# Performance work log

Hardware: AMD Instinct MI355X
Metric: run time of the kernel (lower is better)

Reference implementation:

```python
import jax, jax.numpy as jnp
import numpy as np
import math

N_HEAD = 12
BLOCK = 256  # local attention block size (ls)
EPS = 1e-6


def _rotate(x):
    # pairs (a, b) -> (-b, a) over last dim (matches rotate_embeddings)
    a = x[..., 0::2]
    b = x[..., 1::2]
    return jnp.stack([-b, a], axis=-1).reshape(x.shape)


def setup_inputs() -> dict:
    key = jax.random.key(0)
    k1, k2, k3 = jax.random.split(key, 3)
    B, T, C = 4, 8192, 768
    s = 0.02
    return {
        "x": jax.random.normal(k1, (B, T, C), jnp.float32),
        "w_qkv": jax.random.normal(k2, (C, 3 * C), jnp.float32) * s,
        "w_ln": jnp.ones((C,), jnp.float32),
        "w_proj": jax.random.normal(k3, (C, C), jnp.float32) * s,
    }


def reference(x, w_qkv, w_ln, w_proj):
    B, T, C = x.shape
    nh, ls = N_HEAD, BLOCK
    hd = C // nh
    ng = T // ls

    xb = x.reshape(B, ng, ls, C)
    qkv = xb @ w_qkv                                   # (B,ng,ls,3C)
    q, k, v = jnp.split(qkv, 3, axis=-1)

    # QK RMSNorm over full embedding dim (before head split)
    def rms(t):
        return t * jax.lax.rsqrt(jnp.mean(t * t, axis=-1, keepdims=True) + EPS) * w_ln
    q, k = rms(q), rms(k)

    # split heads: (B,ng,nh,ls,hd)
    def heads(t):
        return jnp.swapaxes(t.reshape(B, ng, ls, nh, hd), 2, 3)
    q, k, v = heads(q), heads(k), heads(v)

    # RoPE (repo layout: freqs tiled via cat((ts,ts)), interleaved pair rotation)
    pos = 10000.0 ** ((-2.0 * jnp.arange(0, hd, 2, dtype=jnp.float32) - 1.0) / hd)
    ts = jnp.arange(ls, dtype=jnp.float32)[:, None] * pos[None, :]   # (ls, hd/2)
    rot = jnp.concatenate([ts, ts], axis=-1)                          # (ls, hd)
    cos, sin = jnp.cos(rot), jnp.sin(rot)
    q = q * cos + _rotate(q) * sin
    k = k * cos + _rotate(k) * sin

    # block-causal scores: causal only within each local block
    scale = 1.0 / math.sqrt(hd)
    att = jnp.einsum('bgnqd,bgnkd->bgnqk', q, k) * scale              # (B,ng,nh,ls,ls)
    mask = jnp.tril(jnp.ones((ls, ls), dtype=bool))
    att = jnp.where(mask, att, -jnp.finfo(att.dtype).max)
    att = jax.nn.softmax(att, axis=-1)
    y = jnp.einsum('bgnqk,bgnkd->bgnqd', att, v)                      # (B,ng,nh,ls,hd)

    y = jnp.swapaxes(y, 2, 3).reshape(B, ng, ls, C)
    y = y @ w_proj
    return y.reshape(B, T, C)
```

## Files before the change

kernel.cpp:

```cpp
#include <hip/hip_runtime.h>
#include <math.h>

typedef __attribute__((ext_vector_type(8))) short bf16x8;
typedef __attribute__((ext_vector_type(4))) short bf16x4;
typedef __attribute__((ext_vector_type(2))) short bf16x2;
typedef __attribute__((ext_vector_type(4))) float f32x4;
typedef __attribute__((ext_vector_type(16))) float f32x16;

#define NH 12
#define HD 64
#define C0 768
#define C3 2304
#define LS 256
#define KT12 12

static __device__ __forceinline__ float bf2f(short u) {
  union { unsigned int i; float f; } c;
  c.i = ((unsigned int)(unsigned short)u) << 16;
  return c.f;
}
static __device__ __forceinline__ short f2bf(float f) {
  union { float f; unsigned int i; } c; c.f = f;
  unsigned int x = c.i;
  x += 0x7fffu + ((x >> 16) & 1u);
  return (short)(x >> 16);
}
static __device__ __forceinline__ unsigned pk2(float a, float b) {
  return (unsigned)(unsigned short)f2bf(a) | ((unsigned)(unsigned short)f2bf(b) << 16);
}

static __device__ __forceinline__ void gload_lds16(const short* g, const short* l) {
  unsigned long long ga = (unsigned long long)g;
  unsigned int la = (unsigned int)(unsigned long long)l;
  __builtin_amdgcn_global_load_lds(
      (const __attribute__((address_space(1))) void*)ga,
      (__attribute__((address_space(3))) void*)la, 16, 0, 0);
}

__global__ __launch_bounds__(256) void cast_kernel(const float* __restrict__ in,
                                                   short* __restrict__ out, int nquads) {
  int i = blockIdx.x * blockDim.x + threadIdx.x;
  int stride = gridDim.x * blockDim.x;
  for (; i < nquads; i += stride) {
    float4 v = ((const float4*)in)[i];
    bf16x4 o = { f2bf(v.x), f2bf(v.y), f2bf(v.z), f2bf(v.w) };
    ((bf16x4*)out)[i] = o;
  }
}

template <int WNG>
__global__ __launch_bounds__(256) void cast_pack_B_kernel(const float* __restrict__ w,
                                                          short* __restrict__ Bpk, int N) {
  __shared__ short sb[WNG * 64 * 64];
  int bn = blockIdx.x, kt = blockIdx.y, t = threadIdx.x;
#pragma unroll
  for (int i = 0; i < WNG * 2; ++i) {
    int seg = i * 256 + t;
    int k = seg / (WNG * 8);
    int nc = (seg % (WNG * 8)) * 8;
    const float* src = w + ((long)(kt * 64 + k)) * N + bn * (WNG * 64) + nc;
    float4 v0 = *(const float4*)src;
    float4 v1 = *(const float4*)(src + 4);
    sb[(nc + 0) * 64 + k] = f2bf(v0.x); sb[(nc + 1) * 64 + k] = f2bf(v0.y);
    sb[(nc + 2) * 64 + k] = f2bf(v0.z); sb[(nc + 3) * 64 + k] = f2bf(v0.w);
    sb[(nc + 4) * 64 + k] = f2bf(v1.x); sb[(nc + 5) * 64 + k] = f2bf(v1.y);
    sb[(nc + 6) * 64 + k] = f2bf(v1.z); sb[(nc + 7) * 64 + k] = f2bf(v1.w);
  }
  __syncthreads();
#pragma unroll
  for (int i = 0; i < WNG * 2; ++i) {
    int c = i * 256 + t;
    int l = c & 63, f = c >> 6;
    int ks = f & 3, nt = (f >> 2) & 1, wng = f >> 3;
    int col = wng * 64 + nt * 32 + (l & 31);
    int kk = ks * 16 + (l >> 5) * 8;
    bf16x8 v = *(bf16x8*)&sb[col * 64 + kk];
    *(bf16x8*)&Bpk[(((long)bn * KT12 + kt) * (WNG * 512) + c) * 8] = v;
  }
}

__global__ void rope_tab_kernel(float* __restrict__ cost, float* __restrict__ sint) {
  int t = blockIdx.x, d = threadIdx.x;
  int i = d & 31;
  float freq = powf(10000.0f, -(float)(4 * i + 1) / 64.0f);
  float th = (float)t * freq;
  cost[t * 64 + d] = cosf(th);
  sint[t * 64 + d] = sinf(th);
}

#define PH_OPEN                                        \
  __builtin_amdgcn_s_barrier();                        \
  asm volatile("s_waitcnt lgkmcnt(0)" ::: "memory");   \
  __builtin_amdgcn_sched_barrier(0);                   \
  __builtin_amdgcn_s_setprio(1);
#define PH_MID __builtin_amdgcn_s_setprio(0);
#define PH_CLOSE                                       \
  asm volatile("s_waitcnt vmcnt(2)" ::: "memory");     \
  __builtin_amdgcn_s_barrier();
#define MM8(ASET, BSET, MP, NT)                                                     \
  { _Pragma("unroll") for (int m2_ = 0; m2_ < 2; ++m2_)                             \
      _Pragma("unroll") for (int ks_ = 0; ks_ < 4; ++ks_)                           \
        acc[(MP)*2 + m2_][NT] = __builtin_amdgcn_mfma_f32_32x32x16_bf16(            \
            ASET[m2_ * 4 + ks_], BSET[ks_], acc[(MP)*2 + m2_][NT], 0, 0, 0); }

template <int OUT_F32, int PACKED_A>
__global__ __launch_bounds__(512, 2) void gemm32_kernel(const short* __restrict__ Apk,
                                                        const short* __restrict__ Bpk,
                                                        const short* __restrict__ Arm,
                                                        void* __restrict__ Cout,
                                                        int N, int K, int nbn) {
  __shared__ short lds[65536];
  int t = threadIdx.x, lane = t & 63, wave = t >> 6;
  int wm = (wave >> 2) * 128, wng = wave & 3, wn = wng * 64, mh = wave >> 2;
  int id = blockIdx.x;
  int cpx = gridDim.x >> 3;
  int sw = (id & 7) * cpx + (id >> 3);
  int bm = sw / nbn, bn = sw % nbn;

  f32x16 acc[4][2];
#pragma unroll
  for (int m = 0; m < 4; ++m)
#pragma unroll
    for (int n = 0; n < 2; ++n)
#pragma unroll
      for (int r = 0; r < 16; ++r) acc[m][n][r] = 0.f;

  bf16x8 a0[8], a1[8], b0[4], b1[4];

  auto STAGE = [&](int s) {
    if (s >= 4 * KT12) return;
    int q = s & 3, Ts = s >> 2;
    int bb = (Ts & 1) * 32768;
    if (q < 2) {
      if (PACKED_A) {
        int c = q * 1024 + t;
        const short* src = Apk + ((long)bm * KT12 + Ts) * 16384 + (long)c * 8;
        gload_lds16(src, &lds[bb + c * 8]);
        gload_lds16(src + 4096, &lds[bb + (c + 512) * 8]);
      } else {
        int row = q * 128 + (t >> 3);
        int cr = q * 1024 + t;
        const short* s1 = Arm + ((long)(bm * 256 + row)) * K + Ts * 64 + ((t & 7) ^ (row & 7)) * 8;
        gload_lds16(s1, &lds[bb + cr * 8]);
        int row2 = row + 64;
        const short* s2 = Arm + ((long)(bm * 256 + row2)) * K + Ts * 64 + ((t & 7) ^ (row2 & 7)) * 8;
        gload_lds16(s2, &lds[bb + (cr + 512) * 8]);
      }
    } else {
      int c = (q - 2) * 1024 + t;
      const short* src = Bpk + ((long)bn * KT12 + Ts) * 16384 + (long)c * 8;
      gload_lds16(src, &lds[bb + 16384 + c * 8]);
      gload_lds16(src + 4096, &lds[bb + 16384 + (c + 512) * 8]);
    }
  };
  auto LDA = [&](bf16x8* d, int b, int mhalf) {
    if (PACKED_A) {
#pragma unroll
      for (int m2 = 0; m2 < 2; ++m2)
#pragma unroll
        for (int ks = 0; ks < 4; ++ks)
          d[m2 * 4 + ks] =
              *(bf16x8*)&lds[b * 32768 + ((mh * 16 + (mhalf * 2 + m2) * 4 + ks) * 64 + lane) * 8];
    } else {
#pragma unroll
      for (int m2 = 0; m2 < 2; ++m2)
#pragma unroll
        for (int ks = 0; ks < 4; ++ks) {
          int row = wm + (mhalf * 2 + m2) * 32 + (lane & 31);
          int g = (ks * 2 + (lane >> 5)) ^ (row & 7);
          d[m2 * 4 + ks] = *(bf16x8*)&lds[b * 32768 + row * 64 + g * 8];
        }
    }
  };
  auto LDB = [&](bf16x8* d, int b, int nt) {
#pragma unroll
    for (int ks = 0; ks < 4; ++ks)
      d[ks] = *(bf16x8*)&lds[b * 32768 + 16384 + ((wng * 8 + nt * 4 + ks) * 64 + lane) * 8];
  };

  for (int s = 0; s < 7; ++s) STAGE(s);
  asm volatile("s_waitcnt vmcnt(6)" ::: "memory");
  __builtin_amdgcn_s_barrier();
  LDA(a0, 0, 0);
  LDB(b0, 0, 0);
  LDB(b1, 0, 1);

  for (int it = 0; it < KT12 / 2; ++it) {
    int P0 = 8 * it;
    PH_OPEN; MM8(a0, b0, 0, 0); PH_MID;
    LDA(a1, 0, 1); STAGE(P0 + 7); PH_CLOSE;
    PH_OPEN; MM8(a0, b1, 0, 1); PH_MID;
    LDA(a0, 1, 0); STAGE(P0 + 8); PH_CLOSE;
    PH_OPEN; MM8(a1, b0, 1, 0); PH_MID;
    LDB(b0, 1, 0); STAGE(P0 + 9); PH_CLOSE;
    PH_OPEN; MM8(a1, b1, 1, 1); PH_MID;
    LDB(b1, 1, 1); STAGE(P0 + 10); PH_CLOSE;
    PH_OPEN; MM8(a0, b0, 0, 0); PH_MID;
    LDA(a1, 1, 1); STAGE(P0 + 11); PH_CLOSE;
    PH_OPEN; MM8(a0, b1, 0, 1); PH_MID;
    LDA(a0, 0, 0); STAGE(P0 + 12); PH_CLOSE;
    PH_OPEN; MM8(a1, b0, 1, 0); PH_MID;
    LDB(b0, 0, 0); STAGE(P0 + 13); PH_CLOSE;
    PH_OPEN; MM8(a1, b1, 1, 1); PH_MID;
    LDB(b1, 0, 1); STAGE(P0 + 14); PH_CLOSE;
  }

  long crow0 = (long)bm * 256 + wm;
  long ccol0 = (long)bn * 256 + wn;
  int rbase = 4 * (lane >> 5);
  int cl = lane & 31;
#pragma unroll
  for (int mt = 0; mt < 4; ++mt)
#pragma unroll
    for (int nt = 0; nt < 2; ++nt)
#pragma unroll
      for (int reg = 0; reg < 16; ++reg) {
        long row = crow0 + mt * 32 + (reg & 3) + 8 * (reg >> 2) + rbase;
        long col = ccol0 + nt * 32 + cl;
        float v = acc[mt][nt][reg];
        if (OUT_F32) ((float*)Cout)[row * N + col] = v;
        else ((short*)Cout)[row * N + col] = f2bf(v);
      }
}

template <int OUT_F32>
__global__ __launch_bounds__(256, 2) void gemm128_kernel(const short* __restrict__ Arm,
                                                         const short* __restrict__ Bpk,
                                                         void* __restrict__ Cout,
                                                         int N, int K, int nbn) {
  __shared__ short lds[32768];
  int t = threadIdx.x, lane = t & 63, wave = t >> 6;
  int wm = (wave >> 1) * 64, wng = wave & 1;
  int id = blockIdx.x;
  int cpx = gridDim.x >> 3;
  int sw = (id & 7) * cpx + (id >> 3);
  int bm = sw / nbn, bn = sw % nbn;
  int l31 = lane & 31, lh = lane >> 5;

  f32x16 acc[2][2];
#pragma unroll
  for (int m = 0; m < 2; ++m)
#pragma unroll
    for (int n = 0; n < 2; ++n)
#pragma unroll
      for (int r = 0; r < 16; ++r) acc[m][n][r] = 0.f;

  auto STAGE = [&](int T) {
    int bb = (T & 1) * 16384;
#pragma unroll
    for (int i = 0; i < 4; ++i) {
      int q = i * 256 + t;
      int row = q >> 3, cp = q & 7;
      const short* ga = Arm + ((long)(bm * 128 + row)) * K + T * 64 + ((cp ^ (row & 7)) * 8);
      gload_lds16(ga, &lds[bb + q * 8]);
      const short* gb = Bpk + ((long)bn * KT12 + T) * 8192 + (long)q * 8;
      gload_lds16(gb, &lds[bb + 8192 + q * 8]);
    }
  };

  STAGE(0);
  asm volatile("s_waitcnt vmcnt(0)" ::: "memory");
  __builtin_amdgcn_s_barrier();

  for (int T = 0; T < KT12; ++T) {
    int bb = (T & 1) * 16384;
    if (T + 1 < KT12) STAGE(T + 1);
    bf16x8 a[2][4], b[2][4];
#pragma unroll
    for (int mt = 0; mt < 2; ++mt) {
      int row = wm + mt * 32 + l31;
      int s8 = row & 7;
#pragma unroll
      for (int ks = 0; ks < 4; ++ks) {
        int g = (ks * 2 + lh) ^ s8;
        a[mt][ks] = *(bf16x8*)&lds[bb + row * 64 + g * 8];
      }
    }
#pragma unroll
    for (int nt = 0; nt < 2; ++nt)
#pragma unroll
      for (int ks = 0; ks < 4; ++ks)
        b[nt][ks] = *(bf16x8*)&lds[bb + 8192 + (((wng * 2 + nt) * 4 + ks) * 64 + lane) * 8];
    __builtin_amdgcn_s_setprio(1);
#pragma unroll
    for (int mt = 0; mt < 2; ++mt)
#pragma unroll
      for (int nt = 0; nt < 2; ++nt)
#pragma unroll
        for (int ks = 0; ks < 4; ++ks)
          acc[mt][nt] = __builtin_amdgcn_mfma_f32_32x32x16_bf16(a[mt][ks], b[nt][ks],
                                                                acc[mt][nt], 0, 0, 0);
    __builtin_amdgcn_s_setprio(0);
    asm volatile("s_waitcnt lgkmcnt(0)" ::: "memory");
    asm volatile("s_waitcnt vmcnt(0)" ::: "memory");
    __builtin_amdgcn_s_barrier();
  }

  long crow0 = (long)bm * 128 + wm;
  long ccol0 = (long)bn * 128 + wng * 64;
  int rbase = 4 * lh;
#pragma unroll
  for (int mt = 0; mt < 2; ++mt)
#pragma unroll
    for (int nt = 0; nt < 2; ++nt)
#pragma unroll
      for (int reg = 0; reg < 16; ++reg) {
        long row = crow0 + mt * 32 + (reg & 3) + 8 * (reg >> 2) + rbase;
        long col = ccol0 + nt * 32 + l31;
        float v = acc[mt][nt][reg];
        if (OUT_F32) ((float*)Cout)[row * N + col] = v;
        else ((short*)Cout)[row * N + col] = f2bf(v);
      }
}

__global__ __launch_bounds__(384) void norm_rope_kernel(short* __restrict__ QKV,
    const float* __restrict__ w_ln, const float* __restrict__ cost,
    const float* __restrict__ sint) {
  int row = blockIdx.x;
  int t = row & 255;
  int i = threadIdx.x;
  bool isq = i < 192;
  int e0 = (i - (isq ? 0 : 192)) * 4;
  long off = (long)row * C3 + (isq ? 0 : C0) + e0;
  bf16x4 v4 = *(const bf16x4*)&QKV[off];
  float a = bf2f(v4.x), b = bf2f(v4.y), c = bf2f(v4.z), d = bf2f(v4.w);
  float ss = a * a + b * b + c * c + d * d;
#pragma unroll
  for (int o = 32; o > 0; o >>= 1) ss += __shfl_down(ss, o);
  __shared__ float red[6];
  if ((i & 63) == 0) red[i >> 6] = ss;
  __syncthreads();
  float s3 = isq ? (red[0] + red[1] + red[2]) : (red[3] + red[4] + red[5]);
  float r = rsqrtf(s3 * (1.0f / 768.0f) + 1e-6f);
  float4 wl = *(const float4*)&w_ln[e0];
  int d0 = e0 & 63;
  float4 cs = *(const float4*)&cost[t * 64 + d0];
  float4 sn = *(const float4*)&sint[t * 64 + d0];
  float n0 = a * r * wl.x, n1 = b * r * wl.y, n2 = c * r * wl.z, n3 = d * r * wl.w;
  bf16x4 o;
  o.x = f2bf(n0 * cs.x - n1 * sn.x);
  o.y = f2bf(n1 * cs.y + n0 * sn.y);
  o.z = f2bf(n2 * cs.z - n3 * sn.z);
  o.w = f2bf(n3 * cs.w + n2 * sn.w);
  *(bf16x4*)&QKV[off] = o;
}

__global__ __launch_bounds__(512, 3) void attn_kernel(const short* __restrict__ QKV,
                                                      short* __restrict__ Y) {
  __shared__ short Ks[256 * 64];
  __shared__ short Vt[64 * 256];
  int blk = blockIdx.x;
  int bg = blk / NH, h = blk % NH;
  const long base = (long)bg * LS * C3 + h * HD;
  int tid = threadIdx.x, lane = tid & 63, wave = tid >> 6;
  int lr = lane & 15, lg = lane >> 4;

#pragma unroll
  for (int it = 0; it < 4; ++it) {
    int q = it * 512 + tid;
    int row = q >> 3, cp = q & 7;
    int gcp = cp ^ (row & 7);
    gload_lds16(QKV + base + (long)row * C3 + C0 + gcp * 8, &Ks[q * 8]);
  }
#pragma unroll
  for (int it = 0; it < 8; ++it) {
    int e = tid * 4 + it * 2048;
    int k = e >> 6, n = e & 63;
    bf16x4 v = *(const bf16x4*)&QKV[base + (long)k * C3 + 2 * C0 + n];
#pragma unroll
    for (int j = 0; j < 4; ++j) {
      int nn = n + j;
      Vt[nn * 256 + (((k >> 3) ^ (nn & 7)) << 3) + (k & 7)] = v[j];
    }
  }
  asm volatile("s_waitcnt vmcnt(0)" ::: "memory");
  __syncthreads();

  int addrA = (((lane >> 4) & 1) * 32 + lr) * 4;
  int addrB = addrA + 64;
  bool selhi = (lane & 32) != 0;

  for (int tt = 0; tt < 2; ++tt) {
    int tile = (tt == 0) ? wave : (15 - wave);
    int m0 = tile * 16;
    bf16x8 qf[2];
#pragma unroll
    for (int ks = 0; ks < 2; ++ks)
      qf[ks] = *(const bf16x8*)&QKV[base + (long)(m0 + lr) * C3 + ks * 32 + lg * 8];

    f32x4 zero4 = {0.f, 0.f, 0.f, 0.f};
    f32x4 accs[16];
#pragma unroll
    for (int n = 0; n < 16; ++n) accs[n] = zero4;

    __builtin_amdgcn_s_setprio(1);
#pragma unroll
    for (int n = 0; n < 16; ++n) {
      if (n <= tile) {
        int row = n * 16 + lr, sw = row & 7;
        bf16x8 k0 = *(bf16x8*)&Ks[row * 64 + ((lg ^ sw) << 3)];
        bf16x8 k1 = *(bf16x8*)&Ks[row * 64 + (((4 + lg) ^ sw) << 3)];
        accs[n] = __builtin_amdgcn_mfma_f32_16x16x32_bf16(k0, qf[0], accs[n], 0, 0, 0);
        accs[n] = __builtin_amdgcn_mfma_f32_16x16x32_bf16(k1, qf[1], accs[n], 0, 0, 0);
      }
    }
    __builtin_amdgcn_s_setprio(0);

    float tm[16];
#pragma unroll
    for (int n = 0; n < 16; ++n) {
      if (n <= tile) {
        if (n == tile) {
#pragma unroll
          for (int r = 0; r < 4; ++r)
            accs[n][r] = (lg * 4 + r <= lr) ? accs[n][r] : -1e30f;
        }
        float m01 = fmaxf(accs[n][0], accs[n][1]);
        float m23 = fmaxf(accs[n][2], accs[n][3]);
        tm[n] = fmaxf(m01, m23);
      } else {
        tm[n] = -1e30f;
      }
    }
#pragma unroll
    for (int st = 1; st < 16; st <<= 1)
#pragma unroll
      for (int j = 0; j < 16; j += 2 * st) tm[j] = fmaxf(tm[j], tm[j + st]);
    float mloc = tm[0];
    mloc = fmaxf(mloc, __shfl_xor(mloc, 16));
    mloc = fmaxf(mloc, __shfl_xor(mloc, 32));

    float ts[16];
#pragma unroll
    for (int n = 0; n < 16; ++n) {
      if (n <= tile) {
#pragma unroll
        for (int r = 0; r < 4; ++r) accs[n][r] = __expf((accs[n][r] - mloc) * 0.125f);
        float s01 = accs[n][0] + accs[n][1];
        float s23 = accs[n][2] + accs[n][3];
        ts[n] = s01 + s23;
      } else {
        ts[n] = 0.f;
      }
    }
#pragma unroll
    for (int st = 1; st < 16; st <<= 1)
#pragma unroll
      for (int j = 0; j < 16; j += 2 * st) ts[j] += ts[j + st];
    float s = ts[0];
    s += __shfl_xor(s, 16);
    s += __shfl_xor(s, 32);
    float rs = 1.0f / s;
    float rv[4];
#pragma unroll
    for (int r = 0; r < 4; ++r) {
      union { float f; int i; } c; c.f = rs;
      union { int i; float f; } o;
      o.i = __builtin_amdgcn_ds_bpermute((lg * 4 + r) * 4, c.i);
      rv[r] = o.f;
    }

    int ktmax = (m0 + 15) >> 5;
    f32x4 yacc[4];
#pragma unroll
    for (int n2 = 0; n2 < 4; ++n2) yacc[n2] = zero4;
#pragma unroll
    for (int kt = 0; kt < 8; ++kt) {
      if (kt <= ktmax) {
        int n0 = 2 * kt, n1 = 2 * kt + 1;
        unsigned a01_0 = pk2(accs[n0][0], accs[n0][1]);
        unsigned a23_0 = pk2(accs[n0][2], accs[n0][3]);
        unsigned a01_1 = (n1 <= tile) ? pk2(accs[n1][0], accs[n1][1]) : 0u;
        unsigned a23_1 = (n1 <= tile) ? pk2(accs[n1][2], accs[n1][3]) : 0u;
        union { unsigned u[4]; bf16x8 v; } af;
        unsigned g0a = (unsigned)__builtin_amdgcn_ds_bpermute(addrA, (int)a01_0);
        unsigned g0b = (unsigned)__builtin_amdgcn_ds_bpermute(addrA, (int)a01_1);
        unsigned g1a = (unsigned)__builtin_amdgcn_ds_bpermute(addrA, (int)a23_0);
        unsigned g1b = (unsigned)__builtin_amdgcn_ds_bpermute(addrA, (int)a23_1);
        unsigned g2a = (unsigned)__builtin_amdgcn_ds_bpermute(addrB, (int)a01_0);
        unsigned g2b = (unsigned)__builtin_amdgcn_ds_bpermute(addrB, (int)a01_1);
        unsigned g3a = (unsigned)__builtin_amdgcn_ds_bpermute(addrB, (int)a23_0);
        unsigned g3b = (unsigned)__builtin_amdgcn_ds_bpermute(addrB, (int)a23_1);
        af.u[0] = selhi ? g0b : g0a;
        af.u[1] = selhi ? g1b : g1a;
        af.u[2] = selhi ? g2b : g2a;
        af.u[3] = selhi ? g3b : g3a;
        int ac = kt * 32 + lg * 8;
        __builtin_amdgcn_s_setprio(1);
#pragma unroll
        for (int n2 = 0; n2 < 4; ++n2) {
          int vn = n2 * 16 + lr;
          bf16x8 vb = *(bf16x8*)&Vt[vn * 256 + (((ac >> 3) ^ (vn & 7)) << 3)];
          yacc[n2] = __builtin_amdgcn_mfma_f32_16x16x32_bf16(af.v, vb, yacc[n2], 0, 0, 0);
        }
        __builtin_amdgcn_s_setprio(0);
      }
    }

#pragma unroll
    for (int n2 = 0; n2 < 4; ++n2) {
#pragma unroll
      for (int r = 0; r < 4; ++r) {
        int row = m0 + lg * 4 + r, d = n2 * 16 + lr;
        Y[((long)(bg * LS + row)) * C0 + h * HD + d] = f2bf(yacc[n2][r] * rv[r]);
      }
    }
  }
}

extern "C" void kernel_launch(void* const* d_in, const int* in_sizes, int n_in,
                              void* d_out, int out_size, void* d_ws, size_t ws_size,
                              hipStream_t stream) {
  (void)in_sizes; (void)n_in; (void)out_size; (void)ws_size;
  const float* x = (const float*)d_in[0];
  const float* w_qkv = (const float*)d_in[1];
  const float* w_ln = (const float*)d_in[2];
  const float* w_proj = (const float*)d_in[3];
  float* out = (float*)d_out;

  char* ws = (char*)d_ws;
  short* Xb      = (short*)(ws + 0);
  short* QKV     = (short*)(ws + 50331648);
  short* Yb      = (short*)(ws + 201326592);
  short* WqkvPk  = (short*)(ws + 251658240);
  short* WprojPk = (short*)(ws + 255197184);
  float* cost    = (float*)(ws + 256376832);
  float* sint    = (float*)(ws + 256442368);

  cast_kernel<<<2048, 256, 0, stream>>>(x, Xb, (4 * 8192 * C0) / 4);
  cast_pack_B_kernel<4><<<dim3(9, KT12), 256, 0, stream>>>(w_qkv, WqkvPk, C3);
  cast_pack_B_kernel<2><<<dim3(6, KT12), 256, 0, stream>>>(w_proj, WprojPk, C0);
  rope_tab_kernel<<<256, 64, 0, stream>>>(cost, sint);

  gemm32_kernel<0, 0><<<128 * 9, 512, 0, stream>>>(nullptr, WqkvPk, Xb, QKV,
                                                   C3, C0, 9);
  norm_rope_kernel<<<32768, 384, 0, stream>>>(QKV, w_ln, cost, sint);
  attn_kernel<<<128 * NH, 512, 0, stream>>>(QKV, Yb);
  gemm128_kernel<1><<<256 * 6, 256, 0, stream>>>(Yb, WprojPk, out, C0, C0, 6);
}
```

Measured before the change: 372.0 us.

## Pre-pack activation tiles into MFMA fragment layout and re-swizzle V transpose

Replaces the plain fp32-to-bf16 cast of x with a kernel that casts and repacks each 256x64 tile into the MFMA fragment order, so the QKV GEMM uses the packed-A path with contiguous LDS loads instead of swizzled row-major loads. The attention kernel now loads V with 16-byte vectors and uses an XOR swizzle that also mixes in the high bits of the column index, aiming to reduce LDS bank conflicts on the transposed V writes. The cast pass gains an LDS round trip, and the packed layout ties A to this tile shape.

New measurement: 362.9 us. 1.03x faster.

```diff
diff --git a/kernel.cpp b/kernel.cpp
--- a/kernel.cpp
+++ b/kernel.cpp
@@ -37,14 +37,31 @@
       (__attribute__((address_space(3))) void*)la, 16, 0, 0);
 }
 
-__global__ __launch_bounds__(256) void cast_kernel(const float* __restrict__ in,
-                                                   short* __restrict__ out, int nquads) {
-  int i = blockIdx.x * blockDim.x + threadIdx.x;
-  int stride = gridDim.x * blockDim.x;
-  for (; i < nquads; i += stride) {
-    float4 v = ((const float4*)in)[i];
-    bf16x4 o = { f2bf(v.x), f2bf(v.y), f2bf(v.z), f2bf(v.w) };
-    ((bf16x4*)out)[i] = o;
+__global__ __launch_bounds__(256) void cast_pack_A_kernel(const float* __restrict__ x,
+                                                          short* __restrict__ Apk) {
+  __shared__ short sb[256 * 64];
+  int bm = blockIdx.x, kt = blockIdx.y, t = threadIdx.x;
+#pragma unroll
+  for (int i = 0; i < 8; ++i) {
+    int seg = i * 256 + t;
+    int row = seg >> 3, sc8 = seg & 7;
+    const float* src = x + ((long)(bm * 256 + row)) * C0 + kt * 64 + sc8 * 8;
+    float4 v0 = *(const float4*)src;
+    float4 v1 = *(const float4*)(src + 4);
+    bf16x8 o = { f2bf(v0.x), f2bf(v0.y), f2bf(v0.z), f2bf(v0.w),
+                 f2bf(v1.x), f2bf(v1.y), f2bf(v1.z), f2bf(v1.w) };
+    *(bf16x8*)&sb[row * 64 + ((sc8 ^ (row & 7)) << 3)] = o;
+  }
+  __syncthreads();
+#pragma unroll
+  for (int i = 0; i < 8; ++i) {
+    int c = i * 256 + t;
+    int l = c & 63, f = c >> 6;
+    int ks = f & 3, mt = (f >> 2) & 3, mh = f >> 4;
+    int row = mh * 128 + mt * 32 + (l & 31);
+    int kc = ks * 2 + (l >> 5);
+    bf16x8 v = *(bf16x8*)&sb[row * 64 + ((kc ^ (row & 7)) << 3)];
+    *(bf16x8*)&Apk[(((long)bm * KT12 + kt) * 2048 + c) * 8] = v;
   }
 }
 
@@ -103,10 +120,9 @@
         acc[(MP)*2 + m2_][NT] = __builtin_amdgcn_mfma_f32_32x32x16_bf16(            \
             ASET[m2_ * 4 + ks_], BSET[ks_], acc[(MP)*2 + m2_][NT], 0, 0, 0); }
 
-template <int OUT_F32, int PACKED_A>
+template <int OUT_F32>
 __global__ __launch_bounds__(512, 2) void gemm32_kernel(const short* __restrict__ Apk,
                                                         const short* __restrict__ Bpk,
-                                                        const short* __restrict__ Arm,
                                                         void* __restrict__ Cout,
                                                         int N, int K, int nbn) {
   __shared__ short lds[65536];
@@ -132,20 +148,10 @@
     int q = s & 3, Ts = s >> 2;
     int bb = (Ts & 1) * 32768;
     if (q < 2) {
-      if (PACKED_A) {
-        int c = q * 1024 + t;
-        const short* src = Apk + ((long)bm * KT12 + Ts) * 16384 + (long)c * 8;
-        gload_lds16(src, &lds[bb + c * 8]);
-        gload_lds16(src + 4096, &lds[bb + (c + 512) * 8]);
-      } else {
-        int row = q * 128 + (t >> 3);
-        int cr = q * 1024 + t;
-        const short* s1 = Arm + ((long)(bm * 256 + row)) * K + Ts * 64 + ((t & 7) ^ (row & 7)) * 8;
-        gload_lds16(s1, &lds[bb + cr * 8]);
-        int row2 = row + 64;
-        const short* s2 = Arm + ((long)(bm * 256 + row2)) * K + Ts * 64 + ((t & 7) ^ (row2 & 7)) * 8;
-        gload_lds16(s2, &lds[bb + (cr + 512) * 8]);
-      }
+      int c = q * 1024 + t;
+      const short* src = Apk + ((long)bm * KT12 + Ts) * 16384 + (long)c * 8;
+      gload_lds16(src, &lds[bb + c * 8]);
+      gload_lds16(src + 4096, &lds[bb + (c + 512) * 8]);
     } else {
       int c = (q - 2) * 1024 + t;
       const short* src = Bpk + ((long)bn * KT12 + Ts) * 16384 + (long)c * 8;
@@ -154,23 +160,12 @@
     }
   };
   auto LDA = [&](bf16x8* d, int b, int mhalf) {
-    if (PACKED_A) {
-#pragma unroll
-      for (int m2 = 0; m2 < 2; ++m2)
-#pragma unroll
-        for (int ks = 0; ks < 4; ++ks)
-          d[m2 * 4 + ks] =
-              *(bf16x8*)&lds[b * 32768 + ((mh * 16 + (mhalf * 2 + m2) * 4 + ks) * 64 + lane) * 8];
-    } else {
-#pragma unroll
-      for (int m2 = 0; m2 < 2; ++m2)
-#pragma unroll
-        for (int ks = 0; ks < 4; ++ks) {
-          int row = wm + (mhalf * 2 + m2) * 32 + (lane & 31);
-          int g = (ks * 2 + (lane >> 5)) ^ (row & 7);
-          d[m2 * 4 + ks] = *(bf16x8*)&lds[b * 32768 + row * 64 + g * 8];
-        }
-    }
+#pragma unroll
+    for (int m2 = 0; m2 < 2; ++m2)
+#pragma unroll
+      for (int ks = 0; ks < 4; ++ks)
+        d[m2 * 4 + ks] =
+            *(bf16x8*)&lds[b * 32768 + ((mh * 16 + (mhalf * 2 + m2) * 4 + ks) * 64 + lane) * 8];
   };
   auto LDB = [&](bf16x8* d, int b, int nt) {
 #pragma unroll
@@ -363,14 +358,15 @@
     gload_lds16(QKV + base + (long)row * C3 + C0 + gcp * 8, &Ks[q * 8]);
   }
 #pragma unroll
-  for (int it = 0; it < 8; ++it) {
-    int e = tid * 4 + it * 2048;
+  for (int it = 0; it < 4; ++it) {
+    int e = tid * 8 + it * 4096;
     int k = e >> 6, n = e & 63;
-    bf16x4 v = *(const bf16x4*)&QKV[base + (long)k * C3 + 2 * C0 + n];
-#pragma unroll
-    for (int j = 0; j < 4; ++j) {
+    bf16x8 v = *(const bf16x8*)&QKV[base + (long)k * C3 + 2 * C0 + n];
+#pragma unroll
+    for (int j = 0; j < 8; ++j) {
       int nn = n + j;
-      Vt[nn * 256 + (((k >> 3) ^ (nn & 7)) << 3) + (k & 7)] = v[j];
+      int key = (nn & 7) ^ (nn >> 3);
+      Vt[nn * 256 + (((k >> 3) ^ key) << 3) + (k & 7)] = v[j];
     }
   }
   asm volatile("s_waitcnt vmcnt(0)" ::: "memory");
@@ -490,7 +486,8 @@
 #pragma unroll
         for (int n2 = 0; n2 < 4; ++n2) {
           int vn = n2 * 16 + lr;
-          bf16x8 vb = *(bf16x8*)&Vt[vn * 256 + (((ac >> 3) ^ (vn & 7)) << 3)];
+          int vkey = (vn & 7) ^ (vn >> 3);
+          bf16x8 vb = *(bf16x8*)&Vt[vn * 256 + (((ac >> 3) ^ vkey) << 3)];
           yacc[n2] = __builtin_amdgcn_mfma_f32_16x16x32_bf16(af.v, vb, yacc[n2], 0, 0, 0);
         }
         __builtin_amdgcn_s_setprio(0);
@@ -519,7 +516,7 @@
   float* out = (float*)d_out;
 
   char* ws = (char*)d_ws;
-  short* Xb      = (short*)(ws + 0);
+  short* Apk     = (short*)(ws + 0);
   short* QKV     = (short*)(ws + 50331648);
   short* Yb      = (short*)(ws + 201326592);
   short* WqkvPk  = (short*)(ws + 251658240);
@@ -527,13 +524,12 @@
   float* cost    = (float*)(ws + 256376832);
   float* sint    = (float*)(ws + 256442368);
 
-  cast_kernel<<<2048, 256, 0, stream>>>(x, Xb, (4 * 8192 * C0) / 4);
+  cast_pack_A_kernel<<<dim3(128, KT12), 256, 0, stream>>>(x, Apk);
   cast_pack_B_kernel<4><<<dim3(9, KT12), 256, 0, stream>>>(w_qkv, WqkvPk, C3);
   cast_pack_B_kernel<2><<<dim3(6, KT12), 256, 0, stream>>>(w_proj, WprojPk, C0);
   rope_tab_kernel<<<256, 64, 0, stream>>>(cost, sint);
 
-  gemm32_kernel<0, 0><<<128 * 9, 512, 0, stream>>>(nullptr, WqkvPk, Xb, QKV,
-                                                   C3, C0, 9);
+  gemm32_kernel<0><<<128 * 9, 512, 0, stream>>>(Apk, WqkvPk, QKV, C3, C0, 9);
   norm_rope_kernel<<<32768, 384, 0, stream>>>(QKV, w_ln, cost, sint);
   attn_kernel<<<128 * NH, 512, 0, stream>>>(QKV, Yb);
   gemm128_kernel<1><<<256 * 6, 256, 0, stream>>>(Yb, WprojPk, out, C0, C0, 6);
```
